# Kernel tuning notes

Measured on AMD Instinct MI355X. Metric: run time of the kernel, lower is better.

Reference implementation:

```python
import jax, jax.numpy as jnp
import numpy as np

N_NODES = 100000
N_EDGES = 1600000
D = 64


def setup_inputs() -> dict:
    key = jax.random.key(0)
    ks = jax.random.split(key, 9)
    x = jax.random.normal(ks[0], (N_NODES, D), dtype=jnp.float32)
    src = jax.random.randint(ks[1], (N_EDGES,), 0, N_NODES, dtype=jnp.int64)
    dst = jax.random.randint(ks[2], (N_EDGES,), 0, N_NODES, dtype=jnp.int64)
    s = 1.0 / np.sqrt(D)
    W_self1 = jax.random.normal(ks[3], (D, D), dtype=jnp.float32) * s
    W_neigh1 = jax.random.normal(ks[4], (D, D), dtype=jnp.float32) * s
    b1 = jnp.zeros((D,), dtype=jnp.float32)
    W_self2 = jax.random.normal(ks[5], (D, D), dtype=jnp.float32) * s
    W_neigh2 = jax.random.normal(ks[6], (D, D), dtype=jnp.float32) * s
    b2 = jnp.zeros((D,), dtype=jnp.float32)
    return {"x": x, "src": src, "dst": dst,
            "W_self1": W_self1, "W_neigh1": W_neigh1, "b1": b1,
            "W_self2": W_self2, "W_neigh2": W_neigh2, "b2": b2}


def _sage_layer(h, src, dst, W_self, W_neigh, b, n_nodes):
    # gather source-node features along edges: [E, d]
    msg = h[src]
    # sum messages into destination nodes, then normalize by in-degree (mean agg)
    agg = jax.ops.segment_sum(msg, dst, num_segments=n_nodes)
    deg = jax.ops.segment_sum(jnp.ones((src.shape[0], 1), h.dtype), dst,
                              num_segments=n_nodes)
    h_neigh = agg / jnp.maximum(deg, 1.0)
    # DGL SAGEConv (mean): fc_self(h) + fc_neigh(h_neigh) + bias
    return h @ W_self + h_neigh @ W_neigh + b


def reference(x, src, dst, W_self1, W_neigh1, b1, W_self2, W_neigh2, b2):
    n = x.shape[0]
    h = _sage_layer(x, src, dst, W_self1, W_neigh1, b1, n)
    # note: source module's forward applies no activation between layers
    h = _sage_layer(h, src, dst, W_self2, W_neigh2, b2, n)
    return h
```

## Files before the change

### kernel.cpp

```cpp
#include <hip/hip_runtime.h>
#include <hip/hip_bf16.h>


#define D 64
#define CAP 64
#define BNODES 256
#define BCAP 4736
#define MAXNB 512

typedef __bf16 bf16x8 __attribute__((ext_vector_type(8)));
typedef float  f32x4  __attribute__((ext_vector_type(4)));

__device__ __forceinline__ unsigned pack2(float a, float b) {
    __hip_bfloat162 t = __float22bfloat162_rn(make_float2(a, b));
    return *(unsigned*)&t;
}
__device__ __forceinline__ unsigned short f2b(float f) {
    __hip_bfloat16 b = __float2bfloat16(f);
    return *(unsigned short*)&b;
}


__global__ void __launch_bounds__(256)
prep_kernel(const float4* __restrict__ x, uint4* __restrict__ xb4,
            unsigned* __restrict__ xsent, unsigned* __restrict__ h1sent,
            const int* __restrict__ src, const int* __restrict__ dst,
            int* __restrict__ gcur, int* __restrict__ gbucket,
            int E, int NB, int n8, int bin_blocks) {
    const int bid = blockIdx.x;
    const int t   = threadIdx.x;

    if (bid < bin_blocks) {
        __shared__ int hist[MAXNB];
        for (int i = t; i < NB; i += 256) hist[i] = 0;
        __syncthreads();

        const int e4_total = E >> 2;
        const int base4    = bid * 1024;

        int4 sv[4], dv[4];
        bool have[4];
        #pragma unroll
        for (int k = 0; k < 4; ++k) {
            int i4 = base4 + t + k * 256;
            have[k] = i4 < e4_total;
            if (have[k]) {
                sv[k] = ((const int4*)src)[i4];
                dv[k] = ((const int4*)dst)[i4];
            }
        }

        #pragma unroll
        for (int k = 0; k < 4; ++k) if (have[k]) {
            atomicAdd(&hist[dv[k].x >> 8], 1);
            atomicAdd(&hist[dv[k].y >> 8], 1);
            atomicAdd(&hist[dv[k].z >> 8], 1);
            atomicAdd(&hist[dv[k].w >> 8], 1);
        }

        int  tail_s = 0, tail_d = 0;
        bool have_tail = false;
        if (bid == 0) {
            int e = (e4_total << 2) + t;
            if (e < E) {
                tail_s = src[e]; tail_d = dst[e]; have_tail = true;
                atomicAdd(&hist[tail_d >> 8], 1);
            }
        }
        __syncthreads();

        for (int i = t; i < NB; i += 256) {
            int c = hist[i];
            hist[i] = (c > 0) ? atomicAdd(&gcur[i], c) : 0;
        }
        __syncthreads();

        #pragma unroll
        for (int k = 0; k < 4; ++k) if (have[k]) {
            int4 s = sv[k], d = dv[k];
            int b, p;
            b = d.x >> 8; p = atomicAdd(&hist[b], 1); if (p < BCAP) gbucket[b * BCAP + p] = ((d.x & 255) << 17) | s.x;
            b = d.y >> 8; p = atomicAdd(&hist[b], 1); if (p < BCAP) gbucket[b * BCAP + p] = ((d.y & 255) << 17) | s.y;
            b = d.z >> 8; p = atomicAdd(&hist[b], 1); if (p < BCAP) gbucket[b * BCAP + p] = ((d.z & 255) << 17) | s.z;
            b = d.w >> 8; p = atomicAdd(&hist[b], 1); if (p < BCAP) gbucket[b * BCAP + p] = ((d.w & 255) << 17) | s.w;
        }
        if (have_tail) {
            int b = tail_d >> 8, p = atomicAdd(&hist[b], 1);
            if (p < BCAP) gbucket[b * BCAP + p] = ((tail_d & 255) << 17) | tail_s;
        }
        return;
    }

    const int cb = bid - bin_blocks;
    const int i  = cb * 256 + t;
    if (i < n8) {
        float4 a = x[2 * i], b = x[2 * i + 1];
        uint4 o;
        o.x = pack2(a.x, a.y);
        o.y = pack2(a.z, a.w);
        o.z = pack2(b.x, b.y);
        o.w = pack2(b.z, b.w);
        xb4[i] = o;
    }
    if (cb == 0 && t < 64) {
        if (t < 32) xsent[t] = 0u;
        else        h1sent[t - 32] = 0u;
    }
}


__global__ void __launch_bounds__(256)
ellify_kernel(const int* __restrict__ gcur, const int* __restrict__ gbucket,
              int* __restrict__ cnt, int* __restrict__ edge_idx, int N) {
    __shared__ int scnt[BNODES];
    scnt[threadIdx.x] = 0;
    __syncthreads();

    const int b     = blockIdx.x;
    const int ne    = min(gcur[b], BCAP);
    const int node0 = b << 8;

    for (int e = threadIdx.x; e < ne; e += 256) {
        int p   = gbucket[b * BCAP + e];
        int s   = p & 0x1FFFF;
        int ld  = p >> 17;
        int pos = atomicAdd(&scnt[ld], 1);
        if (pos < CAP) edge_idx[(size_t)(node0 + ld) * CAP + pos] = s;
    }
    __syncthreads();

    int node = node0 + threadIdx.x;
    if (node < N) {
        int raw = scnt[threadIdx.x];
        cnt[node] = raw;
        int c  = min(raw, CAP);
        int c8 = (c + 7) & ~7;
        for (int p = c; p < c8; ++p)
            edge_idx[(size_t)node * CAP + p] = N;
    }
}


__device__ __forceinline__ void acc8(float& a0, float& a1, float& a2, float& a3,
                                     float& a4, float& a5, float& a6, float& a7,
                                     uint4 u) {
    a0 += __uint_as_float(u.x << 16);
    a1 += __uint_as_float(u.x & 0xffff0000u);
    a2 += __uint_as_float(u.y << 16);
    a3 += __uint_as_float(u.y & 0xffff0000u);
    a4 += __uint_as_float(u.z << 16);
    a5 += __uint_as_float(u.z & 0xffff0000u);
    a6 += __uint_as_float(u.w << 16);
    a7 += __uint_as_float(u.w & 0xffff0000u);
}

__device__ __forceinline__ uint4 gather_row8(const uint4* __restrict__ h4,
                                             const int* __restrict__ cnt,
                                             const int* __restrict__ edge_idx,
                                             int node, int N, int q, int g) {
    const int nodec = (node < N) ? node : (N - 1);
    const int count = (node < N) ? min(cnt[nodec], CAP) : 0;
    const int c8    = (count + 7) & ~7;
    const int start = nodec * CAP;
    const int b0    = g << 3;

    float a0 = 0.f, a1 = 0.f, a2 = 0.f, a3 = 0.f;
    float a4 = 0.f, a5 = 0.f, a6 = 0.f, a7 = 0.f;

    int sreg = edge_idx[start + q];

    for (int j = 0; j < c8; j += 8) {
        const int jn = j + 8;
        const int jc = (jn < c8) ? jn : 0;
        const int sreg_next = edge_idx[start + jc + q];

        const int s0 = __shfl(sreg, b0 + 0, 64);
        const int s1 = __shfl(sreg, b0 + 1, 64);
        const int s2 = __shfl(sreg, b0 + 2, 64);
        const int s3 = __shfl(sreg, b0 + 3, 64);
        const int s4 = __shfl(sreg, b0 + 4, 64);
        const int s5 = __shfl(sreg, b0 + 5, 64);
        const int s6 = __shfl(sreg, b0 + 6, 64);
        const int s7 = __shfl(sreg, b0 + 7, 64);
        uint4 u0 = h4[(size_t)s0 * 8 + q];
        uint4 u1 = h4[(size_t)s1 * 8 + q];
        uint4 u2 = h4[(size_t)s2 * 8 + q];
        uint4 u3 = h4[(size_t)s3 * 8 + q];
        uint4 u4 = h4[(size_t)s4 * 8 + q];
        uint4 u5 = h4[(size_t)s5 * 8 + q];
        uint4 u6 = h4[(size_t)s6 * 8 + q];
        uint4 u7 = h4[(size_t)s7 * 8 + q];

        __builtin_amdgcn_sched_barrier(0);

        acc8(a0, a1, a2, a3, a4, a5, a6, a7, u0);
        acc8(a0, a1, a2, a3, a4, a5, a6, a7, u1);
        acc8(a0, a1, a2, a3, a4, a5, a6, a7, u2);
        acc8(a0, a1, a2, a3, a4, a5, a6, a7, u3);
        acc8(a0, a1, a2, a3, a4, a5, a6, a7, u4);
        acc8(a0, a1, a2, a3, a4, a5, a6, a7, u5);
        acc8(a0, a1, a2, a3, a4, a5, a6, a7, u6);
        acc8(a0, a1, a2, a3, a4, a5, a6, a7, u7);

        sreg = sreg_next;
    }

    const float inv = 1.0f / fmaxf((float)count, 1.0f);
    uint4 o;
    o.x = pack2(a0 * inv, a1 * inv);
    o.y = pack2(a2 * inv, a3 * inv);
    o.z = pack2(a4 * inv, a5 * inv);
    o.w = pack2(a6 * inv, a7 * inv);
    return o;
}

__device__ __forceinline__ bf16x8 cvt8(float4 a, float4 b) {
    union { bf16x8 v; __hip_bfloat162 p[4]; } u;
    u.p[0] = __float22bfloat162_rn(make_float2(a.x, a.y));
    u.p[1] = __float22bfloat162_rn(make_float2(a.z, a.w));
    u.p[2] = __float22bfloat162_rn(make_float2(b.x, b.y));
    u.p[3] = __float22bfloat162_rn(make_float2(b.z, b.w));
    return u.v;
}
__device__ __forceinline__ bf16x8 asbf(uint4 u) {
    union { uint4 a; bf16x8 v; } c; c.a = u; return c.v;
}

__global__ void __launch_bounds__(256, 3)
fused_kernel(const unsigned short* __restrict__ h,
             const int* __restrict__ cnt,
             const int* __restrict__ edge_idx,
             const float* __restrict__ Wself,
             const float* __restrict__ Wneigh,
             const float* __restrict__ bias,
             float* __restrict__ out_f32,
             unsigned short* __restrict__ out_bf16, int N) {
    const int lane = threadIdx.x & 63;
    const int q    = lane & 7;
    const int g    = lane >> 3;
    const int col  = lane & 15;
    const int quad = lane >> 4;
    const int wave = blockIdx.x * (blockDim.x >> 6) + (threadIdx.x >> 6);
    const int n_waves = gridDim.x * (blockDim.x >> 6);

    bf16x8 Bf[4][4];
    #pragma unroll
    for (int nt = 0; nt < 4; ++nt) {
        const int n = nt * 16 + col;
        #pragma unroll
        for (int kk = 0; kk < 4; ++kk) {
            const float* W = (kk < 2) ? Wself : Wneigh;
            const int kbase = (kk & 1) * 32 + quad * 8;
            float w0 = W[(kbase + 0) * D + n];
            float w1 = W[(kbase + 1) * D + n];
            float w2 = W[(kbase + 2) * D + n];
            float w3 = W[(kbase + 3) * D + n];
            float w4 = W[(kbase + 4) * D + n];
            float w5 = W[(kbase + 5) * D + n];
            float w6 = W[(kbase + 6) * D + n];
            float w7 = W[(kbase + 7) * D + n];
            Bf[nt][kk] = cvt8(make_float4(w0, w1, w2, w3), make_float4(w4, w5, w6, w7));
        }
    }

    float bv[4];
    #pragma unroll
    for (int nt = 0; nt < 4; ++nt) bv[nt] = bias[nt * 16 + col];

    const uint4* __restrict__ h4 = (const uint4*)h;

    const int tiles = (N + 15) >> 4;
    for (int t = wave; t < tiles; t += n_waves) {
        uint4 P0 = gather_row8(h4, cnt, edge_idx, t * 16 + g,     N, q, g);

        int row = t * 16 + col;
        if (row >= N) row = N - 1;
        uint4 A0u = h4[(size_t)row * 8 + quad];
        uint4 A1u = h4[(size_t)row * 8 + 4 + quad];

        uint4 P1 = gather_row8(h4, cnt, edge_idx, t * 16 + 8 + g, N, q, g);

        const int srcA2 = ((lane & 7) << 3) + quad;
        const int srcA3 = srcA2 + 4;
        const bool hi   = (lane & 8) != 0;
        uint4 A2u, A3u;
        {
            unsigned l0 = __shfl(P0.x, srcA2, 64), h0 = __shfl(P1.x, srcA2, 64);
            unsigned l1 = __shfl(P0.y, srcA2, 64), h1 = __shfl(P1.y, srcA2, 64);
            unsigned l2 = __shfl(P0.z, srcA2, 64), h2 = __shfl(P1.z, srcA2, 64);
            unsigned l3 = __shfl(P0.w, srcA2, 64), h3 = __shfl(P1.w, srcA2, 64);
            A2u.x = hi ? h0 : l0;  A2u.y = hi ? h1 : l1;
            A2u.z = hi ? h2 : l2;  A2u.w = hi ? h3 : l3;
        }
        {
            unsigned l0 = __shfl(P0.x, srcA3, 64), h0 = __shfl(P1.x, srcA3, 64);
            unsigned l1 = __shfl(P0.y, srcA3, 64), h1 = __shfl(P1.y, srcA3, 64);
            unsigned l2 = __shfl(P0.z, srcA3, 64), h2 = __shfl(P1.z, srcA3, 64);
            unsigned l3 = __shfl(P0.w, srcA3, 64), h3 = __shfl(P1.w, srcA3, 64);
            A3u.x = hi ? h0 : l0;  A3u.y = hi ? h1 : l1;
            A3u.z = hi ? h2 : l2;  A3u.w = hi ? h3 : l3;
        }

        bf16x8 A0 = asbf(A0u), A1 = asbf(A1u);
        bf16x8 A2 = asbf(A2u), A3 = asbf(A3u);

        #pragma unroll
        for (int nt = 0; nt < 4; ++nt) {
            f32x4 acc = {bv[nt], bv[nt], bv[nt], bv[nt]};
            acc = __builtin_amdgcn_mfma_f32_16x16x32_bf16(A0, Bf[nt][0], acc, 0, 0, 0);
            acc = __builtin_amdgcn_mfma_f32_16x16x32_bf16(A1, Bf[nt][1], acc, 0, 0, 0);
            acc = __builtin_amdgcn_mfma_f32_16x16x32_bf16(A2, Bf[nt][2], acc, 0, 0, 0);
            acc = __builtin_amdgcn_mfma_f32_16x16x32_bf16(A3, Bf[nt][3], acc, 0, 0, 0);
            if (out_f32) {
                #pragma unroll
                for (int r = 0; r < 4; ++r) {
                    const int orow = t * 16 + quad * 4 + r;
                    if (orow < N) out_f32[(size_t)orow * D + nt * 16 + col] = acc[r];
                }
            } else {
                #pragma unroll
                for (int r = 0; r < 4; ++r) {
                    const int orow = t * 16 + quad * 4 + r;
                    if (orow < N) out_bf16[(size_t)orow * D + nt * 16 + col] = f2b(acc[r]);
                }
            }
        }
    }
}


extern "C" void kernel_launch(void* const* d_in, const int* in_sizes, int n_in,
                              void* d_out, int out_size, void* d_ws, size_t ws_size,
                              hipStream_t stream) {
    const float* x   = (const float*)d_in[0];
    const int*   src = (const int*)d_in[1];
    const int*   dst = (const int*)d_in[2];
    const float* Ws1 = (const float*)d_in[3];
    const float* Wn1 = (const float*)d_in[4];
    const float* b1  = (const float*)d_in[5];
    const float* Ws2 = (const float*)d_in[6];
    const float* Wn2 = (const float*)d_in[7];
    const float* b2  = (const float*)d_in[8];

    const int N = in_sizes[0] / D;
    const int E = in_sizes[1];

    float* out = (float*)d_out;

    const int NB = (N + BNODES - 1) / BNODES;

    int* gcur      = (int*)d_ws;
    int* cnt       = gcur + 512;
    int* edge_idx  = cnt + N;
    unsigned short* xb   = (unsigned short*)(edge_idx + (size_t)N * CAP);
    unsigned short* h1b  = xb + (size_t)(N + 1) * D;
    int* gbucket   = (int*)(h1b + (size_t)(N + 1) * D);

    const int n8         = N * D / 8;
    const int cvt_blocks = (n8 + 255) / 256;
    const int e4_total   = E >> 2;
    const int bin_blocks = (e4_total + 1023) / 1024 > 0 ? (e4_total + 1023) / 1024 : 1;

    hipMemsetAsync(gcur, 0, 512 * sizeof(int), stream);

    prep_kernel<<<bin_blocks + cvt_blocks, 256, 0, stream>>>(
        (const float4*)x, (uint4*)xb,
        (unsigned*)(xb + (size_t)N * D), (unsigned*)(h1b + (size_t)N * D),
        src, dst, gcur, gbucket, E, NB, n8, bin_blocks);

    ellify_kernel<<<NB, 256, 0, stream>>>(gcur, gbucket, cnt, edge_idx, N);

    const int tiles   = (N + 15) / 16;
    const int fblocks = (tiles + 3) / 4;

    fused_kernel<<<fblocks, 256, 0, stream>>>(xb, cnt, edge_idx, Ws1, Wn1, b1,
                                              nullptr, h1b, N);
    fused_kernel<<<fblocks, 256, 0, stream>>>(h1b, cnt, edge_idx, Ws2, Wn2, b2,
                                              out, nullptr, N);
}
```

Before: 202.6 us.

## Stage bf16 weights in LDS and interleave two-row neighbor gathers

Weights are converted to bf16 once per block into a padded, transposed shared-memory tile and reloaded per tile, instead of being held in 64 VGPRs for the whole kernel. The aim is to cut register pressure and raise occupancy. The two per-tile row gathers (rows g and g+8) are merged into one loop that issues 16 independent loads per iteration, with a sentinel edge row so finished rows read padding instead of branching. This raises memory-level parallelism, but the wider loop holds more live registers and adds LDS reads per tile.

```diff
diff --git a/kernel.cpp b/kernel.cpp
--- a/kernel.cpp
+++ b/kernel.cpp
@@ -7,6 +7,7 @@
 #define BNODES 256
 #define BCAP 4736
 #define MAXNB 512
+#define WT_STRIDE 144
 
 typedef __bf16 bf16x8 __attribute__((ext_vector_type(8)));
 typedef float  f32x4  __attribute__((ext_vector_type(4)));
@@ -24,9 +25,10 @@
 __global__ void __launch_bounds__(256)
 prep_kernel(const float4* __restrict__ x, uint4* __restrict__ xb4,
             unsigned* __restrict__ xsent, unsigned* __restrict__ h1sent,
+            int* __restrict__ esent,
             const int* __restrict__ src, const int* __restrict__ dst,
             int* __restrict__ gcur, int* __restrict__ gbucket,
-            int E, int NB, int n8, int bin_blocks) {
+            int E, int NB, int n8, int bin_blocks, int N) {
     const int bid = blockIdx.x;
     const int t   = threadIdx.x;
 
@@ -102,9 +104,10 @@
         o.w = pack2(b.z, b.w);
         xb4[i] = o;
     }
-    if (cb == 0 && t < 64) {
-        if (t < 32) xsent[t] = 0u;
-        else        h1sent[t - 32] = 0u;
+    if (cb == 0) {
+        if (t < 32)              xsent[t] = 0u;
+        else if (t < 64)         h1sent[t - 32] = 0u;
+        else if (t < 64 + CAP)   esent[t - 64] = N;
     }
 }
 
@@ -154,74 +157,6 @@
     a7 += __uint_as_float(u.w & 0xffff0000u);
 }
 
-__device__ __forceinline__ uint4 gather_row8(const uint4* __restrict__ h4,
-                                             const int* __restrict__ cnt,
-                                             const int* __restrict__ edge_idx,
-                                             int node, int N, int q, int g) {
-    const int nodec = (node < N) ? node : (N - 1);
-    const int count = (node < N) ? min(cnt[nodec], CAP) : 0;
-    const int c8    = (count + 7) & ~7;
-    const int start = nodec * CAP;
-    const int b0    = g << 3;
-
-    float a0 = 0.f, a1 = 0.f, a2 = 0.f, a3 = 0.f;
-    float a4 = 0.f, a5 = 0.f, a6 = 0.f, a7 = 0.f;
-
-    int sreg = edge_idx[start + q];
-
-    for (int j = 0; j < c8; j += 8) {
-        const int jn = j + 8;
-        const int jc = (jn < c8) ? jn : 0;
-        const int sreg_next = edge_idx[start + jc + q];
-
-        const int s0 = __shfl(sreg, b0 + 0, 64);
-        const int s1 = __shfl(sreg, b0 + 1, 64);
-        const int s2 = __shfl(sreg, b0 + 2, 64);
-        const int s3 = __shfl(sreg, b0 + 3, 64);
-        const int s4 = __shfl(sreg, b0 + 4, 64);
-        const int s5 = __shfl(sreg, b0 + 5, 64);
-        const int s6 = __shfl(sreg, b0 + 6, 64);
-        const int s7 = __shfl(sreg, b0 + 7, 64);
-        uint4 u0 = h4[(size_t)s0 * 8 + q];
-        uint4 u1 = h4[(size_t)s1 * 8 + q];
-        uint4 u2 = h4[(size_t)s2 * 8 + q];
-        uint4 u3 = h4[(size_t)s3 * 8 + q];
-        uint4 u4 = h4[(size_t)s4 * 8 + q];
-        uint4 u5 = h4[(size_t)s5 * 8 + q];
-        uint4 u6 = h4[(size_t)s6 * 8 + q];
-        uint4 u7 = h4[(size_t)s7 * 8 + q];
-
-        __builtin_amdgcn_sched_barrier(0);
-
-        acc8(a0, a1, a2, a3, a4, a5, a6, a7, u0);
-        acc8(a0, a1, a2, a3, a4, a5, a6, a7, u1);
-        acc8(a0, a1, a2, a3, a4, a5, a6, a7, u2);
-        acc8(a0, a1, a2, a3, a4, a5, a6, a7, u3);
-        acc8(a0, a1, a2, a3, a4, a5, a6, a7, u4);
-        acc8(a0, a1, a2, a3, a4, a5, a6, a7, u5);
-        acc8(a0, a1, a2, a3, a4, a5, a6, a7, u6);
-        acc8(a0, a1, a2, a3, a4, a5, a6, a7, u7);
-
-        sreg = sreg_next;
-    }
-
-    const float inv = 1.0f / fmaxf((float)count, 1.0f);
-    uint4 o;
-    o.x = pack2(a0 * inv, a1 * inv);
-    o.y = pack2(a2 * inv, a3 * inv);
-    o.z = pack2(a4 * inv, a5 * inv);
-    o.w = pack2(a6 * inv, a7 * inv);
-    return o;
-}
-
-__device__ __forceinline__ bf16x8 cvt8(float4 a, float4 b) {
-    union { bf16x8 v; __hip_bfloat162 p[4]; } u;
-    u.p[0] = __float22bfloat162_rn(make_float2(a.x, a.y));
-    u.p[1] = __float22bfloat162_rn(make_float2(a.z, a.w));
-    u.p[2] = __float22bfloat162_rn(make_float2(b.x, b.y));
-    u.p[3] = __float22bfloat162_rn(make_float2(b.z, b.w));
-    return u.v;
-}
 __device__ __forceinline__ bf16x8 asbf(uint4 u) {
     union { uint4 a; bf16x8 v; } c; c.a = u; return c.v;
 }
@@ -235,6 +170,25 @@
              const float* __restrict__ bias,
              float* __restrict__ out_f32,
              unsigned short* __restrict__ out_bf16, int N) {
+    __shared__ __align__(16) unsigned short wt[64 * WT_STRIDE];
+
+    {
+        const int t    = threadIdx.x;
+        const int krow = t >> 1;
+        const int c0   = (t & 1) * 32;
+        const float* Wrow = (krow < 64) ? (Wself + krow * 64)
+                                        : (Wneigh + (krow - 64) * 64);
+        for (int i = 0; i < 32; i += 4) {
+            float4 w = *(const float4*)(Wrow + c0 + i);
+            const int n0 = c0 + i;
+            wt[(n0 + 0) * WT_STRIDE + krow] = f2b(w.x);
+            wt[(n0 + 1) * WT_STRIDE + krow] = f2b(w.y);
+            wt[(n0 + 2) * WT_STRIDE + krow] = f2b(w.z);
+            wt[(n0 + 3) * WT_STRIDE + krow] = f2b(w.w);
+        }
+    }
+    __syncthreads();
+
     const int lane = threadIdx.x & 63;
     const int q    = lane & 7;
     const int g    = lane >> 3;
@@ -243,42 +197,112 @@
     const int wave = blockIdx.x * (blockDim.x >> 6) + (threadIdx.x >> 6);
     const int n_waves = gridDim.x * (blockDim.x >> 6);
 
-    bf16x8 Bf[4][4];
-    #pragma unroll
-    for (int nt = 0; nt < 4; ++nt) {
-        const int n = nt * 16 + col;
-        #pragma unroll
-        for (int kk = 0; kk < 4; ++kk) {
-            const float* W = (kk < 2) ? Wself : Wneigh;
-            const int kbase = (kk & 1) * 32 + quad * 8;
-            float w0 = W[(kbase + 0) * D + n];
-            float w1 = W[(kbase + 1) * D + n];
-            float w2 = W[(kbase + 2) * D + n];
-            float w3 = W[(kbase + 3) * D + n];
-            float w4 = W[(kbase + 4) * D + n];
-            float w5 = W[(kbase + 5) * D + n];
-            float w6 = W[(kbase + 6) * D + n];
-            float w7 = W[(kbase + 7) * D + n];
-            Bf[nt][kk] = cvt8(make_float4(w0, w1, w2, w3), make_float4(w4, w5, w6, w7));
-        }
-    }
-
     float bv[4];
     #pragma unroll
     for (int nt = 0; nt < 4; ++nt) bv[nt] = bias[nt * 16 + col];
 
     const uint4* __restrict__ h4 = (const uint4*)h;
+    const int SENT = N * CAP;
 
     const int tiles = (N + 15) >> 4;
     for (int t = wave; t < tiles; t += n_waves) {
-        uint4 P0 = gather_row8(h4, cnt, edge_idx, t * 16 + g,     N, q, g);
+        const int nodeA = t * 16 + g;
+        const int nodeB = nodeA + 8;
+        const int cA = (nodeA < N) ? min(cnt[nodeA], CAP) : 0;
+        const int cB = (nodeB < N) ? min(cnt[nodeB], CAP) : 0;
+        const int c8A = (cA + 7) & ~7;
+        const int c8B = (cB + 7) & ~7;
+        const int startA = ((nodeA < N) ? nodeA : 0) * CAP;
+        const int startB = ((nodeB < N) ? nodeB : 0) * CAP;
+        const int cmax = max(c8A, c8B);
+        const int b0   = g << 3;
+
+        float a0 = 0.f, a1 = 0.f, a2 = 0.f, a3 = 0.f;
+        float a4 = 0.f, a5 = 0.f, a6 = 0.f, a7 = 0.f;
+        float b0f = 0.f, b1f = 0.f, b2f = 0.f, b3f = 0.f;
+        float b4f = 0.f, b5f = 0.f, b6f = 0.f, b7f = 0.f;
+
+        int srA = edge_idx[((0 < c8A) ? startA : SENT) + q];
+        int srB = edge_idx[((0 < c8B) ? startB : SENT) + q];
+
+        for (int j = 0; j < cmax; j += 8) {
+            const int jn = j + 8;
+            const int srA_n = edge_idx[((jn < c8A) ? startA + jn : SENT) + q];
+            const int srB_n = edge_idx[((jn < c8B) ? startB + jn : SENT) + q];
+
+            const int sA0 = __shfl(srA, b0 + 0, 64);
+            const int sA1 = __shfl(srA, b0 + 1, 64);
+            const int sA2 = __shfl(srA, b0 + 2, 64);
+            const int sA3 = __shfl(srA, b0 + 3, 64);
+            const int sA4 = __shfl(srA, b0 + 4, 64);
+            const int sA5 = __shfl(srA, b0 + 5, 64);
+            const int sA6 = __shfl(srA, b0 + 6, 64);
+            const int sA7 = __shfl(srA, b0 + 7, 64);
+            const int sB0 = __shfl(srB, b0 + 0, 64);
+            const int sB1 = __shfl(srB, b0 + 1, 64);
+            const int sB2 = __shfl(srB, b0 + 2, 64);
+            const int sB3 = __shfl(srB, b0 + 3, 64);
+            const int sB4 = __shfl(srB, b0 + 4, 64);
+            const int sB5 = __shfl(srB, b0 + 5, 64);
+            const int sB6 = __shfl(srB, b0 + 6, 64);
+            const int sB7 = __shfl(srB, b0 + 7, 64);
+
+            uint4 uA0 = h4[(size_t)sA0 * 8 + q];
+            uint4 uA1 = h4[(size_t)sA1 * 8 + q];
+            uint4 uA2 = h4[(size_t)sA2 * 8 + q];
+            uint4 uA3 = h4[(size_t)sA3 * 8 + q];
+            uint4 uA4 = h4[(size_t)sA4 * 8 + q];
+            uint4 uA5 = h4[(size_t)sA5 * 8 + q];
+            uint4 uA6 = h4[(size_t)sA6 * 8 + q];
+            uint4 uA7 = h4[(size_t)sA7 * 8 + q];
+            uint4 uB0 = h4[(size_t)sB0 * 8 + q];
+            uint4 uB1 = h4[(size_t)sB1 * 8 + q];
+            uint4 uB2 = h4[(size_t)sB2 * 8 + q];
+            uint4 uB3 = h4[(size_t)sB3 * 8 + q];
+            uint4 uB4 = h4[(size_t)sB4 * 8 + q];
+            uint4 uB5 = h4[(size_t)sB5 * 8 + q];
+            uint4 uB6 = h4[(size_t)sB6 * 8 + q];
+            uint4 uB7 = h4[(size_t)sB7 * 8 + q];
+
+            __builtin_amdgcn_sched_barrier(0);
+
+            acc8(a0, a1, a2, a3, a4, a5, a6, a7, uA0);
+            acc8(a0, a1, a2, a3, a4, a5, a6, a7, uA1);
+            acc8(a0, a1, a2, a3, a4, a5, a6, a7, uA2);
+            acc8(a0, a1, a2, a3, a4, a5, a6, a7, uA3);
+            acc8(a0, a1, a2, a3, a4, a5, a6, a7, uA4);
+            acc8(a0, a1, a2, a3, a4, a5, a6, a7, uA5);
+            acc8(a0, a1, a2, a3, a4, a5, a6, a7, uA6);
+            acc8(a0, a1, a2, a3, a4, a5, a6, a7, uA7);
+            acc8(b0f, b1f, b2f, b3f, b4f, b5f, b6f, b7f, uB0);
+            acc8(b0f, b1f, b2f, b3f, b4f, b5f, b6f, b7f, uB1);
+            acc8(b0f, b1f, b2f, b3f, b4f, b5f, b6f, b7f, uB2);
+            acc8(b0f, b1f, b2f, b3f, b4f, b5f, b6f, b7f, uB3);
+            acc8(b0f, b1f, b2f, b3f, b4f, b5f, b6f, b7f, uB4);
+            acc8(b0f, b1f, b2f, b3f, b4f, b5f, b6f, b7f, uB5);
+            acc8(b0f, b1f, b2f, b3f, b4f, b5f, b6f, b7f, uB6);
+            acc8(b0f, b1f, b2f, b3f, b4f, b5f, b6f, b7f, uB7);
+
+            srA = srA_n;
+            srB = srB_n;
+        }
+
+        const float invA = 1.0f / fmaxf((float)cA, 1.0f);
+        const float invB = 1.0f / fmaxf((float)cB, 1.0f);
+        uint4 P0, P1;
+        P0.x = pack2(a0 * invA, a1 * invA);
+        P0.y = pack2(a2 * invA, a3 * invA);
+        P0.z = pack2(a4 * invA, a5 * invA);
+        P0.w = pack2(a6 * invA, a7 * invA);
+        P1.x = pack2(b0f * invB, b1f * invB);
+        P1.y = pack2(b2f * invB, b3f * invB);
+        P1.z = pack2(b4f * invB, b5f * invB);
+        P1.w = pack2(b6f * invB, b7f * invB);
 
         int row = t * 16 + col;
         if (row >= N) row = N - 1;
         uint4 A0u = h4[(size_t)row * 8 + quad];
         uint4 A1u = h4[(size_t)row * 8 + 4 + quad];
-
-        uint4 P1 = gather_row8(h4, cnt, edge_idx, t * 16 + 8 + g, N, q, g);
 
         const int srcA2 = ((lane & 7) << 3) + quad;
         const int srcA3 = srcA2 + 4;
@@ -303,6 +327,21 @@
 
         bf16x8 A0 = asbf(A0u), A1 = asbf(A1u);
         bf16x8 A2 = asbf(A2u), A3 = asbf(A3u);
+
+        __builtin_amdgcn_sched_barrier(0);
+        int ob = 0;
+        asm volatile("" : "+v"(ob));
+        bf16x8 Bf[4][4];
+        #pragma unroll
+        for (int nt = 0; nt < 4; ++nt) {
+            const int n = nt * 16 + col;
+            #pragma unroll
+            for (int kk = 0; kk < 4; ++kk) {
+                const int kcat0 = ((kk >= 2) ? 64 : 0) + (kk & 1) * 32 + quad * 8;
+                const char* p = (const char*)wt + n * (WT_STRIDE * 2) + kcat0 * 2 + ob;
+                Bf[nt][kk] = *(const bf16x8*)p;
+            }
+        }
 
         #pragma unroll
         for (int nt = 0; nt < 4; ++nt) {
@@ -352,7 +391,7 @@
     int* gcur      = (int*)d_ws;
     int* cnt       = gcur + 512;
     int* edge_idx  = cnt + N;
-    unsigned short* xb   = (unsigned short*)(edge_idx + (size_t)N * CAP);
+    unsigned short* xb   = (unsigned short*)(edge_idx + (size_t)(N + 1) * CAP);
     unsigned short* h1b  = xb + (size_t)(N + 1) * D;
     int* gbucket   = (int*)(h1b + (size_t)(N + 1) * D);
 
@@ -366,7 +405,8 @@
     prep_kernel<<<bin_blocks + cvt_blocks, 256, 0, stream>>>(
         (const float4*)x, (uint4*)xb,
         (unsigned*)(xb + (size_t)N * D), (unsigned*)(h1b + (size_t)N * D),
-        src, dst, gcur, gbucket, E, NB, n8, bin_blocks);
+        edge_idx + (size_t)N * CAP,
+        src, dst, gcur, gbucket, E, NB, n8, bin_blocks, N);
 
     ellify_kernel<<<NB, 256, 0, stream>>>(gcur, gbucket, cnt, edge_idx, N);
 
```

Result: no change. 204.0 us (+0.7%).
